# Kernel optimization log

Measured on AMD Instinct MI355X. Metric: run time of the kernel, lower is better.

## Reference

```python
import jax, jax.numpy as jnp
import numpy as np

B, S, H = 1, 1024, 2048
E, I, TOP_K = 64, 768, 8


def setup_inputs() -> dict:
    key = jax.random.key(0)
    k1, k2, k3, k4, k5 = jax.random.split(key, 5)
    std = 0.02
    return {
        "hidden_states": jax.random.normal(k1, (B, S, H), dtype=jnp.float32),
        "router_w": jax.random.normal(k2, (E, H), dtype=jnp.float32) * std,
        "gate_w": jax.random.normal(k3, (E, I, H), dtype=jnp.float32) * std,
        "up_w": jax.random.normal(k4, (E, I, H), dtype=jnp.float32) * std,
        "down_w": jax.random.normal(k5, (E, H, I), dtype=jnp.float32) * std,
    }


def reference(hidden_states, router_w, gate_w, up_w, down_w):
    b, s, h = hidden_states.shape
    x = hidden_states.reshape(-1, h)                     # [T, H]
    T = x.shape[0]

    # Router: softmax in fp32, top-k, renormalize (matches torch source).
    logits = x @ router_w.T                              # [T, E]
    probs = jax.nn.softmax(logits.astype(jnp.float32), axis=-1)
    topk_w, topk_idx = jax.lax.top_k(probs, TOP_K)       # [T, K]
    topk_w = topk_w / jnp.sum(topk_w, axis=-1, keepdims=True)
    topk_w = topk_w.astype(hidden_states.dtype)

    # Dense combine weights: zero for unselected experts. [T, E]
    tok = jnp.arange(T)[:, None]
    combine = jnp.zeros((T, E), dtype=hidden_states.dtype).at[tok, topk_idx].add(topk_w)

    # Scan over experts: SwiGLU MLP on all tokens, weighted-accumulate.
    # Tokens with zero combine weight contribute nothing (same math as the
    # gather/scatter loop in the torch source).
    def body(acc, p):
        gw, uw, dw, cw = p                                # [I,H],[I,H],[H,I],[T]
        hidden = jax.nn.silu(x @ gw.T) * (x @ uw.T)       # [T, I]
        out = hidden @ dw.T                               # [T, H]
        return acc + cw[:, None] * out, None

    init = jnp.zeros_like(x)
    final, _ = jax.lax.scan(body, init, (gate_w, up_w, down_w, combine.T))
    return final.reshape(b, s, h)
```

## Files before the change

kernel.cpp:

```cpp
#include <hip/hip_runtime.h>

#define T_TOK 1024
#define HD    2048
#define NE    64
#define ID    768
#define TOPK  8

typedef __bf16 bf16x8 __attribute__((ext_vector_type(8)));
typedef __bf16 bf16x4 __attribute__((ext_vector_type(4)));
typedef float  f32x4  __attribute__((ext_vector_type(4)));

__device__ __forceinline__ void load_lds16(const void* src, void* lds) {
  __builtin_amdgcn_global_load_lds(
      (const __attribute__((address_space(1))) void*)src,
      (__attribute__((address_space(3))) void*)lds, 16, 0, 0);
}

__global__ __launch_bounds__(256) void router_kernel(
    const float* __restrict__ x, const float* __restrict__ rw,
    unsigned short* __restrict__ xb_u, float* __restrict__ tw,
    int* __restrict__ counts, int* __restrict__ lists)
{
  __shared__ float  sx[HD];
  __shared__ double slog[NE];
  const int t = blockIdx.x;
  const int tid = threadIdx.x;
  __bf16* xb = (__bf16*)xb_u;

  for (int i = tid; i < HD; i += 256) {
    float v = x[(size_t)t * HD + i];
    sx[i] = v;
    xb[(size_t)t * HD + i] = (__bf16)v;
  }
  __syncthreads();

  const int e = tid >> 2, p = tid & 3;
  const float* rwrow = rw + (size_t)e * HD;
  double acc = 0.0;
  for (int k = p; k < HD; k += 4)
    acc += (double)sx[k] * (double)rwrow[k];
  acc += __shfl_xor(acc, 1, 64);
  acc += __shfl_xor(acc, 2, 64);
  if (p == 0) slog[e] = acc;
  __syncthreads();

  if (tid < 64) {
    double v = slog[tid];
    double selv = -1e300; int seli = 0; double gmax = 0.0;
    #pragma unroll
    for (int k = 0; k < TOPK; ++k) {
      double bv = v; int bi = tid;
      #pragma unroll
      for (int off = 32; off >= 1; off >>= 1) {
        double ov = __shfl_xor(bv, off, 64);
        int    oi = __shfl_xor(bi, off, 64);
        if (ov > bv || (ov == bv && oi < bi)) { bv = ov; bi = oi; }
      }
      if (k == 0) gmax = bv;
      if (tid == k) { selv = bv; seli = bi; }
      if (tid == bi) v = -1e300;
    }
    double e_ = (tid < TOPK) ? exp(selv - gmax) : 0.0;
    double s = e_;
    #pragma unroll
    for (int off = 32; off >= 1; off >>= 1) s += __shfl_xor(s, off, 64);
    if (tid < TOPK) {
      int slot = t * TOPK + tid;
      tw[slot] = (float)(e_ / s);
      int pos = atomicAdd(&counts[seli], 1);
      lists[seli * T_TOK + pos] = slot;
    }
  }
}

__global__ __launch_bounds__(512, 4) void gemm1_kernel(
    const unsigned short* __restrict__ xb_u,
    const float* __restrict__ gw, const float* __restrict__ uw,
    const int* __restrict__ counts, const int* __restrict__ lists,
    const unsigned short* __restrict__ zp_u,
    unsigned short* __restrict__ hb_u)
{
  __shared__ __bf16 sA[2][256 * 32];
  __shared__ __bf16 sG[2][64 * 32];
  __shared__ __bf16 sU[2][64 * 32];
  __shared__ int    sSlot[256];

  const __bf16* xb = (const __bf16*)xb_u;
  const __bf16* zp = (const __bf16*)zp_u;
  __bf16* hb = (__bf16*)hb_u;

  const int wg  = blockIdx.x;
  const int idx = wg >> 3;
  const int e   = (wg & 7) * 8 + idx / 12;
  const int n0  = (idx % 12) * 64;

  const int tid  = threadIdx.x;
  const int wid  = tid >> 6;
  const int lane = tid & 63;
  const int n_e  = counts[e];

  const int wrow = tid >> 3;
  const int wqc  = tid & 7;
  const size_t wsrc0 = ((size_t)e * ID + n0 + wrow) * HD + (size_t)wqc * 4;
  const int wds = wrow * 32 + (((wqc >> 1) ^ ((wrow >> 1) & 3)) * 8) + (wqc & 1) * 4;

  for (int m0 = 0; m0 < n_e; m0 += 256) {
    if (tid < 256) sSlot[tid] = (m0 + tid < n_e) ? lists[e * T_TOK + m0 + tid] : -1;
    __syncthreads();

    const __bf16* abase[2];
    #pragma unroll
    for (int j = 0; j < 2; ++j) {
      int r = wid * 32 + j * 16 + (lane >> 2);
      int slot = sSlot[r];
      int cs = (lane & 3) ^ ((r >> 1) & 3);
      abase[j] = (slot >= 0) ? (xb + (size_t)(slot >> 3) * HD + cs * 8)
                             : (zp + cs * 8);
    }

    f32x4 accg[2][4], accu[2][4];
    const f32x4 vzero = {0.f, 0.f, 0.f, 0.f};
    #pragma unroll
    for (int r = 0; r < 2; ++r)
      #pragma unroll
      for (int c = 0; c < 4; ++c) { accg[r][c] = vzero; accu[r][c] = vzero; }

    const int rows_here = n_e - m0 - wid * 32;

    #pragma unroll
    for (int j = 0; j < 2; ++j)
      load_lds16(abase[j], &sA[0][(wid * 32 + j * 16) * 32]);
    f32x4 ga = *(const f32x4*)(gw + wsrc0);
    f32x4 ua = *(const f32x4*)(uw + wsrc0);
    f32x4 gb_, ub_;

#define G1_STEP(KT, BC, BN_, GC, UC, GN, UN)                                      \
    {                                                                             \
      bf16x4 gv, uv;                                                              \
      _Pragma("unroll") for (int q = 0; q < 4; ++q) {                             \
        gv[q] = (__bf16)GC[q]; uv[q] = (__bf16)UC[q];                             \
      }                                                                           \
      *(bf16x4*)&sG[BC][wds] = gv;                                                \
      *(bf16x4*)&sU[BC][wds] = uv;                                                \
      __syncthreads();                                                            \
      if ((KT) + 1 < HD / 32) {                                                   \
        const int k1 = ((KT) + 1) * 32;                                           \
        _Pragma("unroll") for (int j = 0; j < 2; ++j)                             \
          load_lds16(abase[j] + k1, &sA[BN_][(wid * 32 + j * 16) * 32]);          \
        GN = *(const f32x4*)(gw + wsrc0 + (size_t)k1);                            \
        UN = *(const f32x4*)(uw + wsrc0 + (size_t)k1);                            \
      }                                                                           \
      bf16x8 aF[2];                                                               \
      _Pragma("unroll") for (int r = 0; r < 2; ++r) if (r * 16 < rows_here) {     \
        int row = wid * 32 + r * 16 + (lane & 15);                                \
        int ph = (lane >> 4) ^ ((row >> 1) & 3);                                  \
        aF[r] = *(const bf16x8*)&sA[BC][row * 32 + ph * 8];                       \
      }                                                                           \
      _Pragma("unroll") for (int c = 0; c < 4; ++c) {                             \
        int row = c * 16 + (lane & 15);                                           \
        int ph = (lane >> 4) ^ ((row >> 1) & 3);                                  \
        bf16x8 gF = *(const bf16x8*)&sG[BC][row * 32 + ph * 8];                   \
        bf16x8 uF = *(const bf16x8*)&sU[BC][row * 32 + ph * 8];                   \
        _Pragma("unroll") for (int r = 0; r < 2; ++r) if (r * 16 < rows_here) {   \
          accg[r][c] = __builtin_amdgcn_mfma_f32_16x16x32_bf16(aF[r], gF, accg[r][c], 0, 0, 0); \
          accu[r][c] = __builtin_amdgcn_mfma_f32_16x16x32_bf16(aF[r], uF, accu[r][c], 0, 0, 0); \
        }                                                                         \
      }                                                                           \
    }

    for (int it = 0; it < (HD / 32) / 2; ++it) {
      G1_STEP(2 * it,     0, 1, ga,  ua,  gb_, ub_);
      G1_STEP(2 * it + 1, 1, 0, gb_, ub_, ga,  ua);
    }
#undef G1_STEP

    #pragma unroll
    for (int r = 0; r < 2; ++r) if (r * 16 < rows_here) {
      #pragma unroll
      for (int j = 0; j < 4; ++j) {
        int row = wid * 32 + r * 16 + (lane >> 4) * 4 + j;
        if (m0 + row < n_e) {
          int slot = sSlot[row];
          #pragma unroll
          for (int c = 0; c < 4; ++c) {
            float g = accg[r][c][j], u = accu[r][c][j];
            float h = (g / (1.0f + expf(-g))) * u;
            hb[(size_t)slot * ID + (size_t)(n0 + c * 16 + (lane & 15))] = (__bf16)h;
          }
        }
      }
    }
    __syncthreads();
  }
}

__global__ __launch_bounds__(512, 4) void gemm2_kernel(
    const unsigned short* __restrict__ hb_u,
    const float* __restrict__ dw,
    const int* __restrict__ counts, const int* __restrict__ lists,
    const float* __restrict__ tw,
    const unsigned short* __restrict__ zp_u,
    float* __restrict__ out)
{
  __shared__ __bf16 sA[2][256 * 32];
  __shared__ __bf16 sB[2][64 * 32];
  __shared__ int    sSlot[256];

  const __bf16* hbuf = (const __bf16*)hb_u;
  const __bf16* zp   = (const __bf16*)zp_u;

  const int wg  = blockIdx.x;
  const int idx = wg >> 3;
  const int e   = (wg & 7) * 8 + idx / 32;
  const int n0  = (idx % 32) * 64;

  const int tid  = threadIdx.x;
  const int wid  = tid >> 6;
  const int lane = tid & 63;
  const int n_e  = counts[e];

  const int wrow = tid >> 3;
  const int wqc  = tid & 7;
  const size_t wsrc0 = ((size_t)e * HD + n0 + wrow) * ID + (size_t)wqc * 4;
  const int wds = wrow * 32 + (((wqc >> 1) ^ ((wrow >> 1) & 3)) * 8) + (wqc & 1) * 4;

  for (int m0 = 0; m0 < n_e; m0 += 256) {
    if (tid < 256) sSlot[tid] = (m0 + tid < n_e) ? lists[e * T_TOK + m0 + tid] : -1;
    __syncthreads();

    const __bf16* abase[2];
    #pragma unroll
    for (int j = 0; j < 2; ++j) {
      int r = wid * 32 + j * 16 + (lane >> 2);
      int slot = sSlot[r];
      int cs = (lane & 3) ^ ((r >> 1) & 3);
      abase[j] = (slot >= 0) ? (hbuf + (size_t)slot * ID + cs * 8)
                             : (zp + cs * 8);
    }

    f32x4 acc[2][4];
    const f32x4 vzero = {0.f, 0.f, 0.f, 0.f};
    #pragma unroll
    for (int r = 0; r < 2; ++r)
      #pragma unroll
      for (int c = 0; c < 4; ++c) acc[r][c] = vzero;

    const int rows_here = n_e - m0 - wid * 32;

    #pragma unroll
    for (int j = 0; j < 2; ++j)
      load_lds16(abase[j], &sA[0][(wid * 32 + j * 16) * 32]);
    f32x4 da = *(const f32x4*)(dw + wsrc0);
    f32x4 db_;

#define G2_STEP(KT, BC, BN_, DC, DN)                                              \
    {                                                                             \
      bf16x4 dv;                                                                  \
      _Pragma("unroll") for (int q = 0; q < 4; ++q) dv[q] = (__bf16)DC[q];        \
      *(bf16x4*)&sB[BC][wds] = dv;                                                \
      __syncthreads();                                                            \
      if ((KT) + 1 < ID / 32) {                                                   \
        const int k1 = ((KT) + 1) * 32;                                           \
        _Pragma("unroll") for (int j = 0; j < 2; ++j)                             \
          load_lds16(abase[j] + k1, &sA[BN_][(wid * 32 + j * 16) * 32]);          \
        DN = *(const f32x4*)(dw + wsrc0 + (size_t)k1);                            \
      }                                                                           \
      bf16x8 aF[2];                                                               \
      _Pragma("unroll") for (int r = 0; r < 2; ++r) if (r * 16 < rows_here) {     \
        int row = wid * 32 + r * 16 + (lane & 15);                                \
        int ph = (lane >> 4) ^ ((row >> 1) & 3);                                  \
        aF[r] = *(const bf16x8*)&sA[BC][row * 32 + ph * 8];                       \
      }                                                                           \
      _Pragma("unroll") for (int c = 0; c < 4; ++c) {                             \
        int row = c * 16 + (lane & 15);                                           \
        int ph = (lane >> 4) ^ ((row >> 1) & 3);                                  \
        bf16x8 bF = *(const bf16x8*)&sB[BC][row * 32 + ph * 8];                   \
        _Pragma("unroll") for (int r = 0; r < 2; ++r) if (r * 16 < rows_here) {   \
          acc[r][c] = __builtin_amdgcn_mfma_f32_16x16x32_bf16(aF[r], bF, acc[r][c], 0, 0, 0); \
        }                                                                         \
      }                                                                           \
    }

    for (int it = 0; it < (ID / 32) / 2; ++it) {
      G2_STEP(2 * it,     0, 1, da,  db_);
      G2_STEP(2 * it + 1, 1, 0, db_, da);
    }
#undef G2_STEP

    #pragma unroll
    for (int r = 0; r < 2; ++r) if (r * 16 < rows_here) {
      #pragma unroll
      for (int j = 0; j < 4; ++j) {
        int row = wid * 32 + r * 16 + (lane >> 4) * 4 + j;
        if (m0 + row < n_e) {
          int slot = sSlot[row];
          int token = slot >> 3;
          float w = tw[slot];
          #pragma unroll
          for (int c = 0; c < 4; ++c) {
            atomicAdd(out + (size_t)token * HD + (size_t)(n0 + c * 16 + (lane & 15)),
                      w * acc[r][c][j]);
          }
        }
      }
    }
    __syncthreads();
  }
}

extern "C" void kernel_launch(void* const* d_in, const int* in_sizes, int n_in,
                              void* d_out, int out_size, void* d_ws, size_t ws_size,
                              hipStream_t stream) {
  const float* x  = (const float*)d_in[0];
  const float* rw = (const float*)d_in[1];
  const float* gw = (const float*)d_in[2];
  const float* uw = (const float*)d_in[3];
  const float* dw = (const float*)d_in[4];
  float* out = (float*)d_out;

  char* ws = (char*)d_ws;
  const size_t ZP_OFF  = 0;
  const size_t XB_OFF  = 8192;
  const size_t TW_OFF  = XB_OFF + (size_t)T_TOK * HD * 2;
  const size_t CNT_OFF = TW_OFF + (size_t)T_TOK * TOPK * 4;
  const size_t LST_OFF = CNT_OFF + 256;
  const size_t HB_OFF  = LST_OFF + (size_t)NE * T_TOK * 4;

  unsigned short* zp  = (unsigned short*)(ws + ZP_OFF);
  unsigned short* xb  = (unsigned short*)(ws + XB_OFF);
  float*          tw  = (float*)(ws + TW_OFF);
  int*            cnt = (int*)(ws + CNT_OFF);
  int*            lst = (int*)(ws + LST_OFF);
  unsigned short* hb  = (unsigned short*)(ws + HB_OFF);

  hipMemsetAsync(zp, 0, 8192, stream);
  hipMemsetAsync(cnt, 0, 256, stream);
  hipMemsetAsync(d_out, 0, (size_t)T_TOK * HD * sizeof(float), stream);

  router_kernel<<<T_TOK, 256, 0, stream>>>(x, rw, xb, tw, cnt, lst);
  gemm1_kernel<<<768, 512, 0, stream>>>(xb, gw, uw, cnt, lst, zp, hb);
  gemm2_kernel<<<2048, 512, 0, stream>>>(hb, dw, cnt, lst, tw, zp, out);
}
```

Baseline: 504.7 us.

## Triple-buffer MoE GEMM pipelines with explicit waitcnt and halve gemm1 N tile

Both expert GEMM kernels move from double-buffered to triple-buffered LDS staging. Loads are issued two k-steps ahead and gated by explicit s_waitcnt vmcnt counts and raw s_barrier, so global latency is better hidden. gemm1 narrows its N tile from 64 to 32 and splits the gate and up weight loads across the two halves of the block, doubling the grid to 1536 workgroups for more parallelism. The trade-offs are two barriers per k-step, more LDS per block, and hand-counted vmcnt values that must match the issue order exactly or reads will race.

After: 477.8 us. 1.06x faster.

```diff
diff --git a/kernel.cpp b/kernel.cpp
--- a/kernel.cpp
+++ b/kernel.cpp
@@ -15,6 +15,9 @@
       (const __attribute__((address_space(1))) void*)src,
       (__attribute__((address_space(3))) void*)lds, 16, 0, 0);
 }
+
+#define LGKM0 asm volatile("s_waitcnt lgkmcnt(0)" ::: "memory")
+#define BAR() __builtin_amdgcn_s_barrier()
 
 __global__ __launch_bounds__(256) void router_kernel(
     const float* __restrict__ x, const float* __restrict__ rw,
@@ -80,9 +83,8 @@
     const unsigned short* __restrict__ zp_u,
     unsigned short* __restrict__ hb_u)
 {
-  __shared__ __bf16 sA[2][256 * 32];
-  __shared__ __bf16 sG[2][64 * 32];
-  __shared__ __bf16 sU[2][64 * 32];
+  __shared__ __bf16 sA[3][256 * 32];
+  __shared__ __bf16 sW[3][2][32 * 32];
   __shared__ int    sSlot[256];
 
   const __bf16* xb = (const __bf16*)xb_u;
@@ -91,20 +93,52 @@
 
   const int wg  = blockIdx.x;
   const int idx = wg >> 3;
-  const int e   = (wg & 7) * 8 + idx / 12;
-  const int n0  = (idx % 12) * 64;
-
-  const int tid  = threadIdx.x;
-  const int wid  = tid >> 6;
-  const int lane = tid & 63;
-  const int n_e  = counts[e];
-
-  const int wrow = tid >> 3;
-  const int wqc  = tid & 7;
-  const size_t wsrc0 = ((size_t)e * ID + n0 + wrow) * HD + (size_t)wqc * 4;
-  const int wds = wrow * 32 + (((wqc >> 1) ^ ((wrow >> 1) & 3)) * 8) + (wqc & 1) * 4;
+  const int e   = (wg & 7) * 8 + idx / 24;
+  const int n0  = (idx % 24) * 32;
+
+  const int tid = threadIdx.x, wid = tid >> 6, lane = tid & 63;
+  const int n_e = counts[e];
+
+  const int tid4 = tid & 255;
+  const int wrow = tid4 >> 3, wf = tid4 & 7;
+  const float* wsrc = ((wid < 4) ? gw : uw) + ((size_t)e * ID + n0 + wrow) * HD + wf * 4;
+  const int wmi = (wid < 4) ? 0 : 1;
+  const int wds = wrow * 32 + (((wf >> 1) ^ ((wrow >> 1) & 3)) << 3) + (wf & 1) * 4;
+
+#define G1_STEP(VMLIT, BUF, WREG, KNXT, DO_ISSUE)                                 \
+  {                                                                               \
+    asm volatile("s_waitcnt vmcnt(" VMLIT ")" ::: "memory");                      \
+    bf16x4 wv_;                                                                   \
+    _Pragma("unroll") for (int q = 0; q < 4; ++q) wv_[q] = (__bf16)WREG[q];       \
+    *(bf16x4*)&sW[BUF][wmi][wds] = wv_;                                           \
+    LGKM0; BAR();                                                                 \
+    bf16x8 aF_[2], gF_[2], uF_[2];                                                \
+    _Pragma("unroll") for (int r = 0; r < 2; ++r) {                               \
+      int row = wid * 32 + r * 16 + (lane & 15);                                  \
+      int ch = (lane >> 4) ^ ((row >> 1) & 3);                                    \
+      aF_[r] = *(const bf16x8*)&sA[BUF][row * 32 + ch * 8];                       \
+    }                                                                             \
+    _Pragma("unroll") for (int c = 0; c < 2; ++c) {                               \
+      int row = c * 16 + (lane & 15);                                             \
+      int ch = (lane >> 4) ^ ((row >> 1) & 3);                                    \
+      gF_[c] = *(const bf16x8*)&sW[BUF][0][row * 32 + ch * 8];                    \
+      uF_[c] = *(const bf16x8*)&sW[BUF][1][row * 32 + ch * 8];                    \
+    }                                                                             \
+    LGKM0; BAR();                                                                 \
+    if (DO_ISSUE) {                                                               \
+      load_lds16(abase[0] + (KNXT), &sA[BUF][(wid * 32) * 32]);                   \
+      load_lds16(abase[1] + (KNXT), &sA[BUF][(wid * 32 + 16) * 32]);              \
+      WREG = *(const f32x4*)(wsrc + (KNXT));                                      \
+    }                                                                             \
+    _Pragma("unroll") for (int r = 0; r < 2; ++r) if (r * 16 < rows_here)         \
+      _Pragma("unroll") for (int c = 0; c < 2; ++c) {                             \
+        accg[r][c] = __builtin_amdgcn_mfma_f32_16x16x32_bf16(aF_[r], gF_[c], accg[r][c], 0, 0, 0); \
+        accu[r][c] = __builtin_amdgcn_mfma_f32_16x16x32_bf16(aF_[r], uF_[c], accu[r][c], 0, 0, 0); \
+      }                                                                           \
+  }
 
   for (int m0 = 0; m0 < n_e; m0 += 256) {
+    __syncthreads();
     if (tid < 256) sSlot[tid] = (m0 + tid < n_e) ? lists[e * T_TOK + m0 + tid] : -1;
     __syncthreads();
 
@@ -118,61 +152,35 @@
                              : (zp + cs * 8);
     }
 
-    f32x4 accg[2][4], accu[2][4];
+    f32x4 accg[2][2], accu[2][2];
     const f32x4 vzero = {0.f, 0.f, 0.f, 0.f};
     #pragma unroll
     for (int r = 0; r < 2; ++r)
       #pragma unroll
-      for (int c = 0; c < 4; ++c) { accg[r][c] = vzero; accu[r][c] = vzero; }
+      for (int c = 0; c < 2; ++c) { accg[r][c] = vzero; accu[r][c] = vzero; }
 
     const int rows_here = n_e - m0 - wid * 32;
 
-    #pragma unroll
-    for (int j = 0; j < 2; ++j)
-      load_lds16(abase[j], &sA[0][(wid * 32 + j * 16) * 32]);
-    f32x4 ga = *(const f32x4*)(gw + wsrc0);
-    f32x4 ua = *(const f32x4*)(uw + wsrc0);
-    f32x4 gb_, ub_;
-
-#define G1_STEP(KT, BC, BN_, GC, UC, GN, UN)                                      \
-    {                                                                             \
-      bf16x4 gv, uv;                                                              \
-      _Pragma("unroll") for (int q = 0; q < 4; ++q) {                             \
-        gv[q] = (__bf16)GC[q]; uv[q] = (__bf16)UC[q];                             \
-      }                                                                           \
-      *(bf16x4*)&sG[BC][wds] = gv;                                                \
-      *(bf16x4*)&sU[BC][wds] = uv;                                                \
-      __syncthreads();                                                            \
-      if ((KT) + 1 < HD / 32) {                                                   \
-        const int k1 = ((KT) + 1) * 32;                                           \
-        _Pragma("unroll") for (int j = 0; j < 2; ++j)                             \
-          load_lds16(abase[j] + k1, &sA[BN_][(wid * 32 + j * 16) * 32]);          \
-        GN = *(const f32x4*)(gw + wsrc0 + (size_t)k1);                            \
-        UN = *(const f32x4*)(uw + wsrc0 + (size_t)k1);                            \
-      }                                                                           \
-      bf16x8 aF[2];                                                               \
-      _Pragma("unroll") for (int r = 0; r < 2; ++r) if (r * 16 < rows_here) {     \
-        int row = wid * 32 + r * 16 + (lane & 15);                                \
-        int ph = (lane >> 4) ^ ((row >> 1) & 3);                                  \
-        aF[r] = *(const bf16x8*)&sA[BC][row * 32 + ph * 8];                       \
-      }                                                                           \
-      _Pragma("unroll") for (int c = 0; c < 4; ++c) {                             \
-        int row = c * 16 + (lane & 15);                                           \
-        int ph = (lane >> 4) ^ ((row >> 1) & 3);                                  \
-        bf16x8 gF = *(const bf16x8*)&sG[BC][row * 32 + ph * 8];                   \
-        bf16x8 uF = *(const bf16x8*)&sU[BC][row * 32 + ph * 8];                   \
-        _Pragma("unroll") for (int r = 0; r < 2; ++r) if (r * 16 < rows_here) {   \
-          accg[r][c] = __builtin_amdgcn_mfma_f32_16x16x32_bf16(aF[r], gF, accg[r][c], 0, 0, 0); \
-          accu[r][c] = __builtin_amdgcn_mfma_f32_16x16x32_bf16(aF[r], uF, accu[r][c], 0, 0, 0); \
-        }                                                                         \
-      }                                                                           \
-    }
-
-    for (int it = 0; it < (HD / 32) / 2; ++it) {
-      G1_STEP(2 * it,     0, 1, ga,  ua,  gb_, ub_);
-      G1_STEP(2 * it + 1, 1, 0, gb_, ub_, ga,  ua);
-    }
-#undef G1_STEP
+    f32x4 w0, w1, w2;
+    #pragma unroll
+    for (int t = 0; t < 3; ++t) {
+      load_lds16(abase[0] + t * 32, &sA[t][(wid * 32) * 32]);
+      load_lds16(abase[1] + t * 32, &sA[t][(wid * 32 + 16) * 32]);
+    }
+    w0 = *(const f32x4*)(wsrc);
+    w1 = *(const f32x4*)(wsrc + 32);
+    w2 = *(const f32x4*)(wsrc + 64);
+
+    for (int it = 0; it < 20; ++it) {
+      const int t = it * 3;
+      G1_STEP("6", 0, w0, (t + 3) * 32, 1)
+      G1_STEP("6", 1, w1, (t + 4) * 32, 1)
+      G1_STEP("6", 2, w2, (t + 5) * 32, 1)
+    }
+    G1_STEP("6", 0, w0, 63 * 32, 1)
+    G1_STEP("6", 1, w1, 0, 0)
+    G1_STEP("3", 2, w2, 0, 0)
+    G1_STEP("0", 0, w0, 0, 0)
 
     #pragma unroll
     for (int r = 0; r < 2; ++r) if (r * 16 < rows_here) {
@@ -182,7 +190,7 @@
         if (m0 + row < n_e) {
           int slot = sSlot[row];
           #pragma unroll
-          for (int c = 0; c < 4; ++c) {
+          for (int c = 0; c < 2; ++c) {
             float g = accg[r][c][j], u = accu[r][c][j];
             float h = (g / (1.0f + expf(-g))) * u;
             hb[(size_t)slot * ID + (size_t)(n0 + c * 16 + (lane & 15))] = (__bf16)h;
@@ -190,8 +198,8 @@
         }
       }
     }
-    __syncthreads();
-  }
+  }
+#undef G1_STEP
 }
 
 __global__ __launch_bounds__(512, 4) void gemm2_kernel(
@@ -202,8 +210,8 @@
     const unsigned short* __restrict__ zp_u,
     float* __restrict__ out)
 {
-  __shared__ __bf16 sA[2][256 * 32];
-  __shared__ __bf16 sB[2][64 * 32];
+  __shared__ __bf16 sA[3][256 * 32];
+  __shared__ __bf16 sW[3][64 * 32];
   __shared__ int    sSlot[256];
 
   const __bf16* hbuf = (const __bf16*)hb_u;
@@ -214,17 +222,44 @@
   const int e   = (wg & 7) * 8 + idx / 32;
   const int n0  = (idx % 32) * 64;
 
-  const int tid  = threadIdx.x;
-  const int wid  = tid >> 6;
-  const int lane = tid & 63;
-  const int n_e  = counts[e];
-
-  const int wrow = tid >> 3;
-  const int wqc  = tid & 7;
-  const size_t wsrc0 = ((size_t)e * HD + n0 + wrow) * ID + (size_t)wqc * 4;
-  const int wds = wrow * 32 + (((wqc >> 1) ^ ((wrow >> 1) & 3)) * 8) + (wqc & 1) * 4;
+  const int tid = threadIdx.x, wid = tid >> 6, lane = tid & 63;
+  const int n_e = counts[e];
+
+  const int wrow = tid >> 3, wf = tid & 7;
+  const float* wsrc = dw + ((size_t)e * HD + n0 + wrow) * ID + wf * 4;
+  const int wds = wrow * 32 + (((wf >> 1) ^ ((wrow >> 1) & 3)) << 3) + (wf & 1) * 4;
+
+#define G2_STEP(VMLIT, BUF, WREG, KNXT, DO_ISSUE)                                 \
+  {                                                                               \
+    asm volatile("s_waitcnt vmcnt(" VMLIT ")" ::: "memory");                      \
+    bf16x4 wv_;                                                                   \
+    _Pragma("unroll") for (int q = 0; q < 4; ++q) wv_[q] = (__bf16)WREG[q];       \
+    *(bf16x4*)&sW[BUF][wds] = wv_;                                                \
+    LGKM0; BAR();                                                                 \
+    bf16x8 aF_[2], dF_[4];                                                        \
+    _Pragma("unroll") for (int r = 0; r < 2; ++r) {                               \
+      int row = wid * 32 + r * 16 + (lane & 15);                                  \
+      int ch = (lane >> 4) ^ ((row >> 1) & 3);                                    \
+      aF_[r] = *(const bf16x8*)&sA[BUF][row * 32 + ch * 8];                       \
+    }                                                                             \
+    _Pragma("unroll") for (int c = 0; c < 4; ++c) {                               \
+      int row = c * 16 + (lane & 15);                                             \
+      int ch = (lane >> 4) ^ ((row >> 1) & 3);                                    \
+      dF_[c] = *(const bf16x8*)&sW[BUF][row * 32 + ch * 8];                       \
+    }                                                                             \
+    LGKM0; BAR();                                                                 \
+    if (DO_ISSUE) {                                                               \
+      load_lds16(abase[0] + (KNXT), &sA[BUF][(wid * 32) * 32]);                   \
+      load_lds16(abase[1] + (KNXT), &sA[BUF][(wid * 32 + 16) * 32]);              \
+      WREG = *(const f32x4*)(wsrc + (KNXT));                                      \
+    }                                                                             \
+    _Pragma("unroll") for (int r = 0; r < 2; ++r) if (r * 16 < rows_here)         \
+      _Pragma("unroll") for (int c = 0; c < 4; ++c)                               \
+        acc[r][c] = __builtin_amdgcn_mfma_f32_16x16x32_bf16(aF_[r], dF_[c], acc[r][c], 0, 0, 0); \
+  }
 
   for (int m0 = 0; m0 < n_e; m0 += 256) {
+    __syncthreads();
     if (tid < 256) sSlot[tid] = (m0 + tid < n_e) ? lists[e * T_TOK + m0 + tid] : -1;
     __syncthreads();
 
@@ -247,45 +282,25 @@
 
     const int rows_here = n_e - m0 - wid * 32;
 
-    #pragma unroll
-    for (int j = 0; j < 2; ++j)
-      load_lds16(abase[j], &sA[0][(wid * 32 + j * 16) * 32]);
-    f32x4 da = *(const f32x4*)(dw + wsrc0);
-    f32x4 db_;
-
-#define G2_STEP(KT, BC, BN_, DC, DN)                                              \
-    {                                                                             \
-      bf16x4 dv;                                                                  \
-      _Pragma("unroll") for (int q = 0; q < 4; ++q) dv[q] = (__bf16)DC[q];        \
-      *(bf16x4*)&sB[BC][wds] = dv;                                                \
-      __syncthreads();                                                            \
-      if ((KT) + 1 < ID / 32) {                                                   \
-        const int k1 = ((KT) + 1) * 32;                                           \
-        _Pragma("unroll") for (int j = 0; j < 2; ++j)                             \
-          load_lds16(abase[j] + k1, &sA[BN_][(wid * 32 + j * 16) * 32]);          \
-        DN = *(const f32x4*)(dw + wsrc0 + (size_t)k1);                            \
-      }                                                                           \
-      bf16x8 aF[2];                                                               \
-      _Pragma("unroll") for (int r = 0; r < 2; ++r) if (r * 16 < rows_here) {     \
-        int row = wid * 32 + r * 16 + (lane & 15);                                \
-        int ph = (lane >> 4) ^ ((row >> 1) & 3);                                  \
-        aF[r] = *(const bf16x8*)&sA[BC][row * 32 + ph * 8];                       \
-      }                                                                           \
-      _Pragma("unroll") for (int c = 0; c < 4; ++c) {                             \
-        int row = c * 16 + (lane & 15);                                           \
-        int ph = (lane >> 4) ^ ((row >> 1) & 3);                                  \
-        bf16x8 bF = *(const bf16x8*)&sB[BC][row * 32 + ph * 8];                   \
-        _Pragma("unroll") for (int r = 0; r < 2; ++r) if (r * 16 < rows_here) {   \
-          acc[r][c] = __builtin_amdgcn_mfma_f32_16x16x32_bf16(aF[r], bF, acc[r][c], 0, 0, 0); \
-        }                                                                         \
-      }                                                                           \
-    }
-
-    for (int it = 0; it < (ID / 32) / 2; ++it) {
-      G2_STEP(2 * it,     0, 1, da,  db_);
-      G2_STEP(2 * it + 1, 1, 0, db_, da);
-    }
-#undef G2_STEP
+    f32x4 w0, w1, w2;
+    #pragma unroll
+    for (int t = 0; t < 3; ++t) {
+      load_lds16(abase[0] + t * 32, &sA[t][(wid * 32) * 32]);
+      load_lds16(abase[1] + t * 32, &sA[t][(wid * 32 + 16) * 32]);
+    }
+    w0 = *(const f32x4*)(wsrc);
+    w1 = *(const f32x4*)(wsrc + 32);
+    w2 = *(const f32x4*)(wsrc + 64);
+
+    for (int it = 0; it < 7; ++it) {
+      const int t = it * 3;
+      G2_STEP("6", 0, w0, (t + 3) * 32, 1)
+      G2_STEP("6", 1, w1, (t + 4) * 32, 1)
+      G2_STEP("6", 2, w2, (t + 5) * 32, 1)
+    }
+    G2_STEP("6", 0, w0, 0, 0)
+    G2_STEP("3", 1, w1, 0, 0)
+    G2_STEP("0", 2, w2, 0, 0)
 
     #pragma unroll
     for (int r = 0; r < 2; ++r) if (r * 16 < rows_here) {
@@ -304,8 +319,8 @@
         }
       }
     }
-    __syncthreads();
-  }
+  }
+#undef G2_STEP
 }
 
 extern "C" void kernel_launch(void* const* d_in, const int* in_sizes, int n_in,
@@ -338,6 +353,6 @@
   hipMemsetAsync(d_out, 0, (size_t)T_TOK * HD * sizeof(float), stream);
 
   router_kernel<<<T_TOK, 256, 0, stream>>>(x, rw, xb, tw, cnt, lst);
-  gemm1_kernel<<<768, 512, 0, stream>>>(xb, gw, uw, cnt, lst, zp, hb);
+  gemm1_kernel<<<1536, 512, 0, stream>>>(xb, gw, uw, cnt, lst, zp, hb);
   gemm2_kernel<<<2048, 512, 0, stream>>>(hb, dw, cnt, lst, tw, zp, out);
 }
```
